# Kernel tuning notes

Hardware: AMD Instinct MI355X
Metric: run time of the kernel (lower is better)

## Reference

```python
import jax, jax.numpy as jnp
import numpy as np

N = 50000      # nodes
E = 800000     # edges (avg degree 16)
F_IN = 128     # num_node_features
H = 128        # hidden_dim
G = 500        # num graphs in batch


def setup_inputs() -> dict:
    key = jax.random.key(0)
    ks = jax.random.split(key, 20)
    inp = {
        "x": jax.random.normal(ks[0], (N, F_IN), dtype=jnp.float32),
        "edge_index": jax.random.randint(ks[1], (2, E), 0, N, dtype=jnp.int32),
        "batch": jnp.sort(jax.random.randint(ks[2], (N,), 0, G, dtype=jnp.int32)),
    }
    s = 0.05
    # 3 GIN layers: MLP = Linear -> ReLU -> Linear, plus learnable eps (init 0)
    dims = [(F_IN, H), (H, H), (H, H)]
    for i, (din, dout) in enumerate(dims):
        k = jax.random.split(ks[3 + i], 4)
        inp[f"W1_{i}"] = jax.random.normal(k[0], (din, H), dtype=jnp.float32) * s
        inp[f"b1_{i}"] = jnp.zeros((H,), dtype=jnp.float32)
        inp[f"W2_{i}"] = jax.random.normal(k[1], (H, dout), dtype=jnp.float32) * s
        inp[f"b2_{i}"] = jnp.zeros((dout,), dtype=jnp.float32)
        inp[f"eps_{i}"] = jnp.zeros((), dtype=jnp.float32)
    inp["fc_w"] = jax.random.normal(ks[10], (H, 1), dtype=jnp.float32) * s
    inp["fc_b"] = jnp.zeros((1,), dtype=jnp.float32)
    return inp


def _gin_layer(x, src, dst, eps, W1, b1, W2, b2):
    # neighbor sum: scatter-add messages x[src] into dst rows
    agg = jax.ops.segment_sum(x[src], dst, num_segments=N)  # [N, d]
    h = (1.0 + eps) * x + agg
    h = jax.nn.relu(h @ W1 + b1) @ W2 + b2
    return h


def reference(x, edge_index, batch,
              W1_0, b1_0, W2_0, b2_0, eps_0,
              W1_1, b1_1, W2_1, b2_1, eps_1,
              W1_2, b1_2, W2_2, b2_2, eps_2,
              fc_w, fc_b):
    src, dst = edge_index[0], edge_index[1]
    layers = [(eps_0, W1_0, b1_0, W2_0, b2_0),
              (eps_1, W1_1, b1_1, W2_1, b2_1),
              (eps_2, W1_2, b1_2, W2_2, b2_2)]
    h = x
    for i, (eps, W1, b1, W2, b2) in enumerate(layers):
        h = _gin_layer(h, src, dst, eps, W1, b1, W2, b2)
        if i < len(layers) - 1:
            h = jax.nn.relu(h)  # dropout is identity in eval mode
    # global mean pool over graph ids
    sums = jax.ops.segment_sum(h, batch, num_segments=G)          # [G, H]
    counts = jax.ops.segment_sum(jnp.ones((N,), h.dtype), batch, num_segments=G)
    pooled = sums / jnp.maximum(counts, 1.0)[:, None]
    out = pooled @ fc_w + fc_b  # [G, 1]
    return jnp.squeeze(out, axis=-1)  # [G]
```

## Files before the change

### kernel.cpp

```cpp
#include <hip/hip_runtime.h>


#define FEAT 128
#define BCAP 2048
#define CHUNK 10240

typedef short  bf16x8 __attribute__((ext_vector_type(8)));
typedef float  f32x4  __attribute__((ext_vector_type(4)));

__device__ inline unsigned short f2bf(float f) {
    unsigned int u = __float_as_uint(f);
    u = (u + 0x7FFFu + ((u >> 16) & 1u)) >> 16;
    return (unsigned short)u;
}
__device__ inline float2 bfpair(unsigned int u) {
    float2 r;
    r.x = __uint_as_float(u << 16);
    r.y = __uint_as_float(u & 0xffff0000u);
    return r;
}

__global__ __launch_bounds__(1024) void bucket_kernel(
    const int* __restrict__ src, const int* __restrict__ dst,
    int* __restrict__ bcnt, unsigned int* __restrict__ bpairs, int E) {
    __shared__ unsigned int lpairs[CHUNK];
    __shared__ int lbase[1025];
    __shared__ int lcur[1024];
    __shared__ int lres[1024];
    __shared__ int part[1024];
    int tid = threadIdx.x;
    int e0 = blockIdx.x * CHUNK;
    int e1 = e0 + CHUNK; if (e1 > E) e1 = E;
    int cnt = e1 - e0;
    lcur[tid] = 0;
    __syncthreads();
    for (int e = e0 + tid; e < e1; e += 1024) atomicAdd(&lcur[dst[e] >> 6], 1);
    __syncthreads();
    int v = lcur[tid];
    part[tid] = v;
    __syncthreads();
    for (int d = 1; d < 1024; d <<= 1) {
        int u = (tid >= d) ? part[tid - d] : 0;
        __syncthreads();
        part[tid] += u;
        __syncthreads();
    }
    int ex = part[tid] - v;
    lbase[tid] = ex;
    if (tid == 1023) lbase[1024] = part[1023];
    lcur[tid] = ex;
    lres[tid] = (v > 0) ? atomicAdd(&bcnt[tid * 16], v) : 0;
    __syncthreads();
    for (int e = e0 + tid; e < e1; e += 1024) {
        int d = dst[e], s = src[e];
        int p = atomicAdd(&lcur[d >> 6], 1);
        lpairs[p] = ((unsigned int)s << 6) | (unsigned int)(d & 63);
    }
    __syncthreads();
    for (int j = tid; j < cnt; j += 1024) {
        int lo = 0, hi = 1023;
        while (lo < hi) { int m = (lo + hi + 1) >> 1; if (lbase[m] <= j) lo = m; else hi = m - 1; }
        int gpos = lres[lo] + (j - lbase[lo]);
        if (gpos < BCAP) bpairs[(size_t)lo * BCAP + gpos] = lpairs[j];
    }
}

__global__ __launch_bounds__(256) void deg_kernel(const int* __restrict__ bcnt,
                                                  const unsigned int* __restrict__ bpairs,
                                                  int* __restrict__ off, int n) {
    __shared__ int lh[64];
    int b = blockIdx.x, tid = threadIdx.x;
    if (tid < 64) lh[tid] = 0;
    __syncthreads();
    int cnt = bcnt[b * 16]; if (cnt > BCAP) cnt = BCAP;
    const unsigned int* bp = bpairs + (size_t)b * BCAP;
    for (int i = tid; i < cnt; i += 256) atomicAdd(&lh[bp[i] & 63u], 1);
    __syncthreads();
    if (tid < 64) {
        int node = b * 64 + tid;
        if (node < n) off[node] = lh[tid];
    }
}

__global__ void block_sum_kernel(const int* __restrict__ off, int* __restrict__ bs, int n) {
    int b = blockIdx.x, t = threadIdx.x;
    int base = b * 1024;
    int s = 0;
    #pragma unroll
    for (int i = 0; i < 4; ++i) {
        int idx = base + t + 256 * i;
        if (idx < n) s += off[idx];
    }
    #pragma unroll
    for (int d = 32; d; d >>= 1) s += __shfl_down(s, d, 64);
    __shared__ int ws[4];
    if ((t & 63) == 0) ws[t >> 6] = s;
    __syncthreads();
    if (t == 0) bs[b] = ws[0] + ws[1] + ws[2] + ws[3];
}

__global__ void scan_blocksums_kernel(int* __restrict__ bs, int nb,
                                      int* __restrict__ off, int n) {
    __shared__ int l[1024];
    int t = threadIdx.x;
    int v = (t < nb) ? bs[t] : 0;
    l[t] = v;
    __syncthreads();
    for (int d = 1; d < 1024; d <<= 1) {
        int u = (t >= d) ? l[t - d] : 0;
        __syncthreads();
        l[t] += u;
        __syncthreads();
    }
    if (t < nb) bs[t] = (t == 0) ? 0 : l[t - 1];
    if (t == 1023) off[n] = l[1023];
}

__global__ __launch_bounds__(256) void block_scan_kernel(
    int* __restrict__ off, const int* __restrict__ bs, int n) {
    __shared__ int l[1024];
    __shared__ int part[256];
    int b = blockIdx.x, t = threadIdx.x;
    int base = b * 1024;
    #pragma unroll
    for (int i = 0; i < 4; ++i) {
        int idx = base + t + 256 * i;
        l[t + 256 * i] = (idx < n) ? off[idx] : 0;
    }
    __syncthreads();
    int v0 = l[4 * t], v1 = l[4 * t + 1], v2 = l[4 * t + 2], v3 = l[4 * t + 3];
    int p = v0 + v1 + v2 + v3;
    part[t] = p;
    __syncthreads();
    for (int d = 1; d < 256; d <<= 1) {
        int u = (t >= d) ? part[t - d] : 0;
        __syncthreads();
        part[t] += u;
        __syncthreads();
    }
    int ex = bs[b] + ((t == 0) ? 0 : part[t - 1]);
    int e0 = ex, e1 = ex + v0, e2 = e1 + v1, e3 = e2 + v2;
    int idx = base + 4 * t;
    if (idx + 3 < n) {
        ((int4*)(off + idx))[0] = make_int4(e0, e1, e2, e3);
    } else {
        if (idx + 0 < n) off[idx + 0] = e0;
        if (idx + 1 < n) off[idx + 1] = e1;
        if (idx + 2 < n) off[idx + 2] = e2;
    }
}

__global__ __launch_bounds__(256) void bucket_scatter_kernel(
    const int* __restrict__ bcnt, const unsigned int* __restrict__ bpairs,
    const int* __restrict__ off, int* __restrict__ srcs, int n) {
    __shared__ int lcur[64];
    int b = blockIdx.x, tid = threadIdx.x;
    if (tid < 64) {
        int node = b * 64 + tid;
        lcur[tid] = (node < n) ? off[node] : 0;
    }
    __syncthreads();
    int cnt = bcnt[b * 16]; if (cnt > BCAP) cnt = BCAP;
    const unsigned int* bp = bpairs + (size_t)b * BCAP;
    for (int i = tid; i < cnt; i += 256) {
        unsigned int pr = bp[i];
        int pos = atomicAdd(&lcur[pr & 63u], 1);
        srcs[pos] = (int)(pr >> 6);
    }
}

__global__ __launch_bounds__(256) void setup_kernel(
    const float* __restrict__ x, unsigned int* __restrict__ xbf, long pairs, int nxb,
    const int* __restrict__ batch, int* __restrict__ gstart, int n, int G,
    const float* __restrict__ W2f, const float* __restrict__ b2f,
    const float* __restrict__ fcw, float* __restrict__ weff,
    const float* __restrict__ W0, const float* __restrict__ W1,
    const float* __restrict__ W2, const float* __restrict__ W3,
    const float* __restrict__ W4, unsigned short* __restrict__ Wswz) {
    int b = blockIdx.x, tid = threadIdx.x;
    if (b < nxb) {
        long i = (long)b * 256 + tid;
        if (i < pairs) {
            float2 v = ((const float2*)x)[i];
            unsigned int pk = (unsigned int)f2bf(v.x) | ((unsigned int)f2bf(v.y) << 16);
            long node = i >> 6;
            int dg = (int)(i & 63);
            int slice = dg >> 3, d = dg & 7;
            xbf[(size_t)slice * n * 8 + node * 8 + d] = pk;
        }
    } else if (b < nxb + 2) {
        int i = (b - nxb) * 256 + tid;
        if (i <= G) {
            int lo = 0, hi = n;
            while (lo < hi) { int m = (lo + hi) >> 1; if (batch[m] < i) lo = m + 1; else hi = m; }
            gstart[i] = lo;
        }
    } else if (b == nxb + 2) {
        int lane = tid & 63, wave = tid >> 6;
        float2 f2 = ((const float2*)fcw)[lane];
        for (int r = wave; r < 128; r += 4) {
            float2 w = ((const float2*)(W2f + r * FEAT))[lane];
            float d = w.x * f2.x + w.y * f2.y;
            #pragma unroll
            for (int s = 32; s; s >>= 1) d += __shfl_down(d, s, 64);
            if (lane == 0) weff[r] = d;
        }
        if (wave == 0) {
            float2 bb = ((const float2*)b2f)[lane];
            float d = bb.x * f2.x + bb.y * f2.y;
            #pragma unroll
            for (int s = 32; s; s >>= 1) d += __shfl_down(d, s, 64);
            if (lane == 0) weff[128] = d;
        }
    } else {
        int gid = (b - nxb - 3) * 256 + tid;
        if (gid < 5 * 2048) {
            int mat = gid >> 11;
            int task = gid & 2047;
            int c = task >> 4, m = task & 15;
            const float* W = (mat == 0) ? W0 : (mat == 1) ? W1 : (mat == 2) ? W2 :
                             (mat == 3) ? W3 : W4;
            unsigned short* dp = Wswz + mat * 16384 + c * 128 + ((m ^ (c & 7)) << 3);
            #pragma unroll
            for (int j = 0; j < 8; ++j) dp[j] = f2bf(W[(8 * m + j) * FEAT + c]);
        }
    }
}

__global__ __launch_bounds__(256) void agg_kernel(
    const unsigned int* __restrict__ hs, const int* __restrict__ off,
    const int* __restrict__ srcs, const float* __restrict__ eps_p,
    unsigned int* __restrict__ pre, int n) {
    int b = blockIdx.x;
    int slice = b & 7;
    int chunk = b >> 3;
    int tid = threadIdx.x;
    int wave = tid >> 6, lane = tid & 63;
    int g = lane >> 3, d = lane & 7;
    int node = chunk * 32 + wave * 8 + g;
    if (node >= n) return;
    float eps1 = 1.0f + eps_p[0];
    const unsigned int* hb = hs + (size_t)slice * n * 8;
    float2 self = bfpair(hb[(size_t)node * 8 + d]);
    float2 acc0 = make_float2(self.x * eps1, self.y * eps1);
    float2 acc1 = make_float2(0.f, 0.f);
    float2 acc2 = make_float2(0.f, 0.f);
    float2 acc3 = make_float2(0.f, 0.f);
    int j0 = off[node], j1 = off[node + 1];
    int j = j0;
    for (; j + 4 <= j1; j += 4) {
        int s0 = srcs[j], s1 = srcs[j + 1], s2 = srcs[j + 2], s3 = srcs[j + 3];
        unsigned int u0 = hb[(size_t)s0 * 8 + d];
        unsigned int u1 = hb[(size_t)s1 * 8 + d];
        unsigned int u2 = hb[(size_t)s2 * 8 + d];
        unsigned int u3 = hb[(size_t)s3 * 8 + d];
        float2 v0 = bfpair(u0), v1 = bfpair(u1), v2 = bfpair(u2), v3 = bfpair(u3);
        acc0.x += v0.x; acc0.y += v0.y;  acc1.x += v1.x; acc1.y += v1.y;
        acc2.x += v2.x; acc2.y += v2.y;  acc3.x += v3.x; acc3.y += v3.y;
    }
    for (; j < j1; ++j) {
        int s = srcs[j];
        float2 v = bfpair(hb[(size_t)s * 8 + d]);
        acc0.x += v.x; acc0.y += v.y;
    }
    acc0.x += acc1.x + acc2.x;
    acc0.y += acc1.y + acc2.y;
    acc0.x += acc3.x;
    acc0.y += acc3.y;
    pre[(size_t)slice * n * 8 + (size_t)node * 8 + d] =
        (unsigned int)f2bf(acc0.x) | ((unsigned int)f2bf(acc0.y) << 16);
}

template <int MODE>
__global__ __launch_bounds__(256) void mfma_mlp_kernel(
    const unsigned short* __restrict__ A, const unsigned short* __restrict__ Wswz,
    const float* __restrict__ bias, unsigned short* __restrict__ outbf,
    const int* __restrict__ batch, const float* __restrict__ weff,
    float* __restrict__ sums, int n) {
    __shared__ int4 Wl4[2048];
    int tid = threadIdx.x;
    const int4* ws4 = (const int4*)Wswz;
    #pragma unroll
    for (int i = 0; i < 8; ++i) Wl4[i * 256 + tid] = ws4[i * 256 + tid];
    __syncthreads();
    const unsigned short* Wl = (const unsigned short*)Wl4;

    int lane = tid & 63, wave = tid >> 6;
    int q = lane >> 4, c15 = lane & 15;
    int r0 = blockIdx.x * 64 + wave * 16;
    int arow = r0 + c15;
    bool rv = arow < n;
    size_t sstride = (size_t)n * 16;
    const unsigned short* abase = A + (size_t)arow * 16 + 8 * (q & 1) + (q >> 1) * sstride;

    f32x4 zf = {0.f, 0.f, 0.f, 0.f};
    f32x4 acc[8];
    #pragma unroll
    for (int i = 0; i < 8; ++i) acc[i] = zf;
    bf16x8 zero8 = {0, 0, 0, 0, 0, 0, 0, 0};

    #pragma unroll
    for (int k0 = 0; k0 < 4; ++k0) {
        bf16x8 a = rv ? *(const bf16x8*)(abase + 2 * k0 * sstride) : zero8;
        int m = k0 * 4 + q;
        #pragma unroll
        for (int nt = 0; nt < 8; ++nt) {
            int col = nt * 16 + c15;
            bf16x8 bfr = *(const bf16x8*)&Wl[col * 128 + ((m ^ (col & 7)) << 3)];
            acc[nt] = __builtin_amdgcn_mfma_f32_16x16x32_bf16(a, bfr, acc[nt], 0, 0, 0);
        }
    }

    int orow0 = r0 + q * 4;
    if (MODE == 1) {
        #pragma unroll
        for (int nt = 0; nt < 8; ++nt) {
            float bv = bias[nt * 16 + c15];
            #pragma unroll
            for (int r = 0; r < 4; ++r) {
                int ro = orow0 + r;
                if (ro < n) {
                    float v = fmaxf(acc[nt][r] + bv, 0.f);
                    outbf[(size_t)nt * sstride + (size_t)ro * 16 + c15] = f2bf(v);
                }
            }
        }
    } else {
        __shared__ float gsum[64];
        int r0b = blockIdx.x * 64;
        int lastn = r0b + 63 < n - 1 ? r0b + 63 : n - 1;
        int gmin = batch[r0b];
        int gmax = batch[lastn];
        int span = gmax - gmin + 1;
        bool lds_ok = (span <= 64);
        if (lds_ok) for (int i = tid; i < span; i += 256) gsum[i] = 0.f;
        __syncthreads();
        float rowdot[4] = {0.f, 0.f, 0.f, 0.f};
        #pragma unroll
        for (int nt = 0; nt < 8; ++nt) {
            int col = nt * 16 + c15;
            float bv = bias[col];
            float wv = weff[col];
            #pragma unroll
            for (int r = 0; r < 4; ++r)
                rowdot[r] += fmaxf(acc[nt][r] + bv, 0.f) * wv;
        }
        #pragma unroll
        for (int r = 0; r < 4; ++r) {
            float v = rowdot[r];
            v += __shfl_xor(v, 1, 64);
            v += __shfl_xor(v, 2, 64);
            v += __shfl_xor(v, 4, 64);
            v += __shfl_xor(v, 8, 64);
            if (c15 == 0) {
                int node = orow0 + r;
                if (node < n) {
                    int g = batch[node];
                    if (lds_ok) atomicAdd(&gsum[g - gmin], v);
                    else        atomicAdd(&sums[g], v);
                }
            }
        }
        __syncthreads();
        if (lds_ok)
            for (int i = tid; i < span; i += 256) atomicAdd(&sums[gmin + i], gsum[i]);
    }
}

__global__ void finalize_kernel(const float* __restrict__ sums, const int* __restrict__ gstart,
                                const float* __restrict__ weff, const float* __restrict__ fcb,
                                float* __restrict__ out, int G) {
    int g = blockIdx.x * blockDim.x + threadIdx.x;
    if (g >= G) return;
    int cnt = gstart[g + 1] - gstart[g];
    out[g] = (cnt > 0) ? sums[g] / (float)cnt + weff[128] + fcb[0] : fcb[0];
}

static inline size_t align256(size_t x) { return (x + 255) & ~(size_t)255; }

extern "C" void kernel_launch(void* const* d_in, const int* in_sizes, int n_in,
                              void* d_out, int out_size, void* d_ws, size_t ws_size,
                              hipStream_t stream) {
    const float* x      = (const float*)d_in[0];
    const int*   ei     = (const int*)d_in[1];
    const int*   batch  = (const int*)d_in[2];
    const float* W1[3]  = {(const float*)d_in[3],  (const float*)d_in[8],  (const float*)d_in[13]};
    const float* b1[3]  = {(const float*)d_in[4],  (const float*)d_in[9],  (const float*)d_in[14]};
    const float* W2[3]  = {(const float*)d_in[5],  (const float*)d_in[10], (const float*)d_in[15]};
    const float* b2[3]  = {(const float*)d_in[6],  (const float*)d_in[11], (const float*)d_in[16]};
    const float* eps[3] = {(const float*)d_in[7],  (const float*)d_in[12], (const float*)d_in[17]};
    const float* fcw    = (const float*)d_in[18];
    const float* fcb    = (const float*)d_in[19];
    float* out = (float*)d_out;

    const int N = in_sizes[0] / FEAT;
    const int E = in_sizes[1] / 2;
    const int G = out_size;
    const int nbuckets = (N + 63) >> 6;

    char* p = (char*)d_ws;
    int* off    = (int*)p;  p += align256((size_t)(N + 1) * 4);
    int* srcs   = (int*)p;  p += align256((size_t)E * 4);
    int* bsums  = (int*)p;  p += align256((size_t)1024 * 4);
    int* gstart = (int*)p;  p += align256((size_t)(G + 1) * 4);
    float* weff = (float*)p; p += align256((size_t)256 * 4);
    unsigned short* Wswz = (unsigned short*)p; p += align256((size_t)5 * 16384 * 2);
    float* sums = (float*)p;
    char* z0 = (char*)sums;
    p += align256((size_t)G * 4);
    int* bcnt = (int*)p; p += align256((size_t)nbuckets * 16 * 4);
    size_t zbytes = (size_t)(p - z0);
    unsigned int* bpairs = (unsigned int*)p;     p += align256((size_t)nbuckets * BCAP * 4);
    unsigned int* x_bf   = (unsigned int*)p;     p += align256((size_t)N * 64 * 4);
    unsigned int* pre_bf = (unsigned int*)p;     p += align256((size_t)N * 64 * 4);
    unsigned int* t_bf   = (unsigned int*)p;     p += align256((size_t)N * 64 * 4);
    unsigned int* h_bf   = (unsigned int*)p;     p += align256((size_t)N * 64 * 4);
    (void)ws_size; (void)n_in;

    const int* src = ei;
    const int* dst = ei + E;

    hipMemsetAsync(z0, 0, zbytes, stream);

    const int nb = (N + 1023) / 1024;
    const int nchunks = (E + CHUNK - 1) / CHUNK;
    bucket_kernel<<<nchunks, 1024, 0, stream>>>(src, dst, bcnt, bpairs, E);
    deg_kernel<<<nbuckets, 256, 0, stream>>>(bcnt, bpairs, off, N);
    block_sum_kernel<<<nb, 256, 0, stream>>>(off, bsums, N);
    scan_blocksums_kernel<<<1, 1024, 0, stream>>>(bsums, nb, off, N);
    block_scan_kernel<<<nb, 256, 0, stream>>>(off, bsums, N);
    bucket_scatter_kernel<<<nbuckets, 256, 0, stream>>>(bcnt, bpairs, off, srcs, N);

    long pairs = (long)N * 64;
    int nxb = (int)((pairs + 255) / 256);
    setup_kernel<<<nxb + 43, 256, 0, stream>>>(
        x, x_bf, pairs, nxb, batch, gstart, N, G,
        W2[2], b2[2], fcw, weff,
        W1[0], W2[0], W1[1], W2[1], W1[2], Wswz);

    const int aggBlocks  = 8 * ((N + 31) / 32);
    const int gemmBlocks = (N + 63) / 64;
    const unsigned short* Wz[5] = {Wswz, Wswz + 16384, Wswz + 2 * 16384,
                                   Wswz + 3 * 16384, Wswz + 4 * 16384};

    const unsigned int* h = x_bf;
    for (int i = 0; i < 2; ++i) {
        agg_kernel<<<aggBlocks, 256, 0, stream>>>(h, off, srcs, eps[i], pre_bf, N);
        mfma_mlp_kernel<1><<<gemmBlocks, 256, 0, stream>>>(
            (const unsigned short*)pre_bf, Wz[2 * i], b1[i], (unsigned short*)t_bf,
            nullptr, nullptr, nullptr, N);
        mfma_mlp_kernel<1><<<gemmBlocks, 256, 0, stream>>>(
            (const unsigned short*)t_bf, Wz[2 * i + 1], b2[i], (unsigned short*)h_bf,
            nullptr, nullptr, nullptr, N);
        h = h_bf;
    }
    agg_kernel<<<aggBlocks, 256, 0, stream>>>(h, off, srcs, eps[2], pre_bf, N);
    mfma_mlp_kernel<2><<<gemmBlocks, 256, 0, stream>>>(
        (const unsigned short*)pre_bf, Wz[4], b1[2], nullptr,
        batch, weff, sums, N);

    finalize_kernel<<<(G + 255) / 256, 256, 0, stream>>>(sums, gstart, weff, fcb, out, G);
}
```

Measured before the change: 335.8 us.

## Widen feature slices to 32 bf16 columns and gather uint2 per lane

Changes the sliced bf16 activation layout from 8 slices of 16 features to 4 slices of 32 features, consistently in the setup conversion, the aggregation kernel, and the MFMA GEMM loads and stores. The aggregation kernel now gathers 8 bytes per lane per neighbor (64B per node row) with an 8-way unrolled edge loop, halving the number of aggregation blocks. This aims to raise bytes per gathered transaction and memory-level parallelism in the edge-gather-bound aggregation, at the cost of more registers per thread and fewer blocks.

After: 304.7 us. -9.3%, faster.

```diff
diff --git a/kernel.cpp b/kernel.cpp
--- a/kernel.cpp
+++ b/kernel.cpp
@@ -185,8 +185,8 @@
             unsigned int pk = (unsigned int)f2bf(v.x) | ((unsigned int)f2bf(v.y) << 16);
             long node = i >> 6;
             int dg = (int)(i & 63);
-            int slice = dg >> 3, d = dg & 7;
-            xbf[(size_t)slice * n * 8 + node * 8 + d] = pk;
+            int slice = dg >> 4, d = dg & 15;
+            xbf[(size_t)slice * n * 16 + node * 16 + d] = pk;
         }
     } else if (b < nxb + 2) {
         int i = (b - nxb) * 256 + tid;
@@ -232,43 +232,60 @@
     const int* __restrict__ srcs, const float* __restrict__ eps_p,
     unsigned int* __restrict__ pre, int n) {
     int b = blockIdx.x;
-    int slice = b & 7;
-    int chunk = b >> 3;
+    int slice = b & 3;
+    int chunk = b >> 2;
     int tid = threadIdx.x;
     int wave = tid >> 6, lane = tid & 63;
     int g = lane >> 3, d = lane & 7;
     int node = chunk * 32 + wave * 8 + g;
     if (node >= n) return;
     float eps1 = 1.0f + eps_p[0];
-    const unsigned int* hb = hs + (size_t)slice * n * 8;
-    float2 self = bfpair(hb[(size_t)node * 8 + d]);
-    float2 acc0 = make_float2(self.x * eps1, self.y * eps1);
-    float2 acc1 = make_float2(0.f, 0.f);
-    float2 acc2 = make_float2(0.f, 0.f);
-    float2 acc3 = make_float2(0.f, 0.f);
+    const uint2* hb = (const uint2*)(hs + (size_t)slice * n * 16);
+    uint2 su = hb[(size_t)node * 8 + d];
+    float2 sa = bfpair(su.x), sb = bfpair(su.y);
+    float4 acc0 = make_float4(sa.x * eps1, sa.y * eps1, sb.x * eps1, sb.y * eps1);
+    float4 acc1 = make_float4(0.f, 0.f, 0.f, 0.f);
+    float4 acc2 = make_float4(0.f, 0.f, 0.f, 0.f);
+    float4 acc3 = make_float4(0.f, 0.f, 0.f, 0.f);
     int j0 = off[node], j1 = off[node + 1];
     int j = j0;
+    #define ACC(A, U) { float2 p0 = bfpair(U.x), p1 = bfpair(U.y); \
+        A.x += p0.x; A.y += p0.y; A.z += p1.x; A.w += p1.y; }
+    for (; j + 8 <= j1; j += 8) {
+        int s0 = srcs[j], s1 = srcs[j + 1], s2 = srcs[j + 2], s3 = srcs[j + 3];
+        int s4 = srcs[j + 4], s5 = srcs[j + 5], s6 = srcs[j + 6], s7 = srcs[j + 7];
+        uint2 u0 = hb[(size_t)s0 * 8 + d];
+        uint2 u1 = hb[(size_t)s1 * 8 + d];
+        uint2 u2 = hb[(size_t)s2 * 8 + d];
+        uint2 u3 = hb[(size_t)s3 * 8 + d];
+        uint2 u4 = hb[(size_t)s4 * 8 + d];
+        uint2 u5 = hb[(size_t)s5 * 8 + d];
+        uint2 u6 = hb[(size_t)s6 * 8 + d];
+        uint2 u7 = hb[(size_t)s7 * 8 + d];
+        ACC(acc0, u0) ACC(acc1, u1) ACC(acc2, u2) ACC(acc3, u3)
+        ACC(acc0, u4) ACC(acc1, u5) ACC(acc2, u6) ACC(acc3, u7)
+    }
     for (; j + 4 <= j1; j += 4) {
         int s0 = srcs[j], s1 = srcs[j + 1], s2 = srcs[j + 2], s3 = srcs[j + 3];
-        unsigned int u0 = hb[(size_t)s0 * 8 + d];
-        unsigned int u1 = hb[(size_t)s1 * 8 + d];
-        unsigned int u2 = hb[(size_t)s2 * 8 + d];
-        unsigned int u3 = hb[(size_t)s3 * 8 + d];
-        float2 v0 = bfpair(u0), v1 = bfpair(u1), v2 = bfpair(u2), v3 = bfpair(u3);
-        acc0.x += v0.x; acc0.y += v0.y;  acc1.x += v1.x; acc1.y += v1.y;
-        acc2.x += v2.x; acc2.y += v2.y;  acc3.x += v3.x; acc3.y += v3.y;
+        uint2 u0 = hb[(size_t)s0 * 8 + d];
+        uint2 u1 = hb[(size_t)s1 * 8 + d];
+        uint2 u2 = hb[(size_t)s2 * 8 + d];
+        uint2 u3 = hb[(size_t)s3 * 8 + d];
+        ACC(acc0, u0) ACC(acc1, u1) ACC(acc2, u2) ACC(acc3, u3)
     }
     for (; j < j1; ++j) {
-        int s = srcs[j];
-        float2 v = bfpair(hb[(size_t)s * 8 + d]);
-        acc0.x += v.x; acc0.y += v.y;
-    }
-    acc0.x += acc1.x + acc2.x;
-    acc0.y += acc1.y + acc2.y;
-    acc0.x += acc3.x;
-    acc0.y += acc3.y;
-    pre[(size_t)slice * n * 8 + (size_t)node * 8 + d] =
-        (unsigned int)f2bf(acc0.x) | ((unsigned int)f2bf(acc0.y) << 16);
+        uint2 u = hb[(size_t)srcs[j] * 8 + d];
+        ACC(acc0, u)
+    }
+    #undef ACC
+    acc0.x += acc1.x + acc2.x;  acc0.y += acc1.y + acc2.y;
+    acc0.z += acc1.z + acc2.z;  acc0.w += acc1.w + acc2.w;
+    acc0.x += acc3.x;  acc0.y += acc3.y;
+    acc0.z += acc3.z;  acc0.w += acc3.w;
+    uint2 o;
+    o.x = (unsigned int)f2bf(acc0.x) | ((unsigned int)f2bf(acc0.y) << 16);
+    o.y = (unsigned int)f2bf(acc0.z) | ((unsigned int)f2bf(acc0.w) << 16);
+    ((uint2*)(pre + (size_t)slice * n * 16))[(size_t)node * 8 + d] = o;
 }
 
 template <int MODE>
@@ -290,8 +307,8 @@
     int r0 = blockIdx.x * 64 + wave * 16;
     int arow = r0 + c15;
     bool rv = arow < n;
-    size_t sstride = (size_t)n * 16;
-    const unsigned short* abase = A + (size_t)arow * 16 + 8 * (q & 1) + (q >> 1) * sstride;
+    size_t sstride = (size_t)n * 32;
+    const unsigned short* abase = A + (size_t)arow * 32 + 8 * q;
 
     f32x4 zf = {0.f, 0.f, 0.f, 0.f};
     f32x4 acc[8];
@@ -301,7 +318,7 @@
 
     #pragma unroll
     for (int k0 = 0; k0 < 4; ++k0) {
-        bf16x8 a = rv ? *(const bf16x8*)(abase + 2 * k0 * sstride) : zero8;
+        bf16x8 a = rv ? *(const bf16x8*)(abase + (size_t)k0 * sstride) : zero8;
         int m = k0 * 4 + q;
         #pragma unroll
         for (int nt = 0; nt < 8; ++nt) {
@@ -316,12 +333,13 @@
         #pragma unroll
         for (int nt = 0; nt < 8; ++nt) {
             float bv = bias[nt * 16 + c15];
+            size_t sb = (size_t)(nt >> 1) * sstride + (nt & 1) * 16 + c15;
             #pragma unroll
             for (int r = 0; r < 4; ++r) {
                 int ro = orow0 + r;
                 if (ro < n) {
                     float v = fmaxf(acc[nt][r] + bv, 0.f);
-                    outbf[(size_t)nt * sstride + (size_t)ro * 16 + c15] = f2bf(v);
+                    outbf[sb + (size_t)ro * 32] = f2bf(v);
                 }
             }
         }
@@ -438,7 +456,7 @@
         W2[2], b2[2], fcw, weff,
         W1[0], W2[0], W1[1], W2[1], W1[2], Wswz);
 
-    const int aggBlocks  = 8 * ((N + 31) / 32);
+    const int aggBlocks  = 4 * ((N + 31) / 32);
     const int gemmBlocks = (N + 63) / 64;
     const unsigned short* Wz[5] = {Wswz, Wswz + 16384, Wswz + 2 * 16384,
                                    Wswz + 3 * 16384, Wswz + 4 * 16384};
```
